# Kernel tuning notes

Hardware: AMD Instinct MI355X
Metric: run time of the kernel (lower is better)

## Reference

```python
import jax, jax.numpy as jnp
import numpy as np

DIM = 512
L = 4096
B, H, W = 8, 64, 64
EPS = 1e-06
BN_EPS = 1e-05


def setup_inputs() -> dict:
    key = jax.random.key(0)
    ks = jax.random.split(key, 16)
    s = 1.0 / np.sqrt(DIM)
    d = {
        'x': jax.random.normal(ks[0], (B, DIM, H, W), dtype=jnp.float32),
        'pos_emb': jax.random.normal(ks[1], (1, L, DIM), dtype=jnp.float32),
        'Wq': jax.random.uniform(ks[2], (DIM, DIM), jnp.float32, -s, s),
        'bq': jax.random.uniform(ks[3], (DIM,), jnp.float32, -s, s),
        'Wk': jax.random.uniform(ks[4], (DIM, DIM), jnp.float32, -s, s),
        'bk': jax.random.uniform(ks[5], (DIM,), jnp.float32, -s, s),
        'Wv': jax.random.uniform(ks[6], (DIM, DIM), jnp.float32, -s, s),
        'bv': jax.random.uniform(ks[7], (DIM,), jnp.float32, -s, s),
        'Wq1': jax.random.uniform(ks[8], (DIM, DIM), jnp.float32, -s, s),
        'bq1': jax.random.uniform(ks[9], (DIM,), jnp.float32, -s, s),
        'Wk1': jax.random.uniform(ks[10], (DIM, DIM), jnp.float32, -s, s),
        'bk1': jax.random.uniform(ks[11], (DIM,), jnp.float32, -s, s),
        'gamma': jax.random.normal(ks[12], (1,), jnp.float32) * 0.1,
        'bn_weight': jnp.ones((DIM,), jnp.float32),
        'bn_bias': jnp.zeros((DIM,), jnp.float32),
    }
    return d


def reference(x, pos_emb, Wq, bq, Wk, bk, Wv, bv, Wq1, bq1, Wk1, bk1, gamma, bn_weight, bn_bias):
    Bb, C, Hh, Ww = x.shape
    # [B,C,H,W] -> [B, L, C] tokens
    xs = x.transpose(0, 2, 3, 1).reshape(Bb, Hh * Ww, C) + pos_emb
    Q = jax.nn.relu(xs @ Wq.T + bq)   # kernel_fun = ReLU
    K = jax.nn.relu(xs @ Wk.T + bk)
    V = xs @ Wv.T + bv
    Q1 = xs @ Wq1.T + bq1
    K1 = xs @ Wk1.T + bk1
    # torch einsum 'blc,bcc,bl->blc' uses only diag(KV); compute it directly:
    # diagKV[b,c] = sum_l K[b,l,c] * V[b,l,c]
    diagKV = jnp.einsum('blc,blc->bc', K, V)
    Ksum = K.sum(axis=1)  # == K^T summed over last axis, [B,C]
    Z = 1.0 / jnp.einsum('blc,bc->bl', Q, Ksum + EPS)
    result = Q * diagKV[:, None, :] * Z[:, :, None]  # [B,L,C]
    # channel-softmax attention: softmax over last dim of Q1^T @ K1, [B,C,C]
    mid = jax.nn.softmax(jnp.einsum('blc,bld->bcd', Q1, K1), axis=-1)
    result = result @ mid  # [B,L,C]
    xs = xs + gamma * result
    y = xs.transpose(0, 2, 1).reshape(Bb, C, Hh, Ww)
    # BatchNorm2d in training mode (fresh module): batch stats, biased variance
    mean = y.mean(axis=(0, 2, 3))
    var = y.var(axis=(0, 2, 3))
    yn = (y - mean[None, :, None, None]) * jax.lax.rsqrt(var + BN_EPS)[None, :, None, None]
    yn = yn * bn_weight[None, :, None, None] + bn_bias[None, :, None, None]
    return jax.nn.relu(yn)
```

## Files before the change

### kernel.cpp

```cpp
#include <hip/hip_runtime.h>
#include <stdint.h>

typedef float f32x4 __attribute__((ext_vector_type(4)));
typedef short bf16x8 __attribute__((ext_vector_type(8)));

__device__ __forceinline__ float bf2f(unsigned short h){
  union { unsigned int u; float f; } v; v.u = ((unsigned int)h) << 16; return v.f;
}
__device__ __forceinline__ unsigned short f2bf(float f){
  union { float f; unsigned int u; } v; v.f = f;
  return (unsigned short)((v.u + 0x7fffu + ((v.u >> 16) & 1u)) >> 16);
}

typedef __attribute__((address_space(1))) const unsigned int ga_u32;
typedef __attribute__((address_space(3))) unsigned int ls_u32;
__device__ __forceinline__ void async_load16(const void* g, void* l){
  __builtin_amdgcn_global_load_lds((ga_u32*)g, (ls_u32*)l, 16, 0, 0);
}

#define CFENCE() asm volatile("" ::: "memory")
#define SB0() __builtin_amdgcn_sched_barrier(0)

__global__ __launch_bounds__(256) void k_prep_all(
    const float* __restrict__ w0, const float* __restrict__ w1,
    const float* __restrict__ w2, const float* __restrict__ w3,
    const float* __restrict__ w4,
    const float* __restrict__ b0, const float* __restrict__ b1,
    const float* __restrict__ b2, const float* __restrict__ b3,
    const float* __restrict__ b4,
    unsigned short* __restrict__ wbf, float* __restrict__ bias5,
    unsigned short* __restrict__ wq1x2)
{
  const int bid = blockIdx.x;
  const int t = threadIdx.x;
  if (bid < 5120){
    int slot = bid >> 10;
    int i = (bid & 1023) * 256 + t;
    const float* w = (slot == 0) ? w0 : (slot == 1) ? w1 :
                     (slot == 2) ? w2 : (slot == 3) ? w3 : w4;
    wbf[(size_t)slot * 262144 + i] = f2bf(w[i]);
  } else if (bid < 5130){
    int i = (bid - 5120) * 256 + t;
    int s = i >> 9, r = i & 511;
    const float* b = (s == 0) ? b0 : (s == 1) ? b1 : (s == 2) ? b2 :
                     (s == 3) ? b3 : b4;
    bias5[i] = b[r];
  } else {
    int e = bid - 5130;
    #pragma unroll
    for (int rep = 0; rep < 2; rep++){
      int idx = rep*256 + t;
      unsigned short v = f2bf(w3[e*512 + idx]);
      wq1x2[(size_t)e*1024 + idx] = v;
      wq1x2[(size_t)e*1024 + 512 + idx] = v;
    }
  }
}

__global__ __launch_bounds__(256) void k_build_xs(
    const float* __restrict__ x, const float* __restrict__ pos,
    unsigned short* __restrict__ xsb, unsigned short* __restrict__ xsT,
    float* __restrict__ svec)
{
  __shared__ float tile[64][65];
  __shared__ unsigned short tile2[64][72];
  __shared__ float sred[256];
  const int lt = blockIdx.x, ct = blockIdx.y;
  const int t = threadIdx.x;
  const int rr = t >> 3, c8 = (t & 7) * 8;
  float pr[16];
  #pragma unroll
  for (int pass = 0; pass < 2; pass++){
    int gl = lt*64 + rr + pass*32;
    f32x4 p0 = *(const f32x4*)(pos + (size_t)gl * 512 + ct*64 + c8);
    f32x4 p1 = *(const f32x4*)(pos + (size_t)gl * 512 + ct*64 + c8 + 4);
    #pragma unroll
    for (int s = 0; s < 4; s++){ pr[pass*8+s] = p0[s]; pr[pass*8+4+s] = p1[s]; }
  }
  for (int b = 0; b < 8; b++){
    #pragma unroll
    for (int pass = 0; pass < 2; pass++){
      int r = rr + pass * 32;
      const float* src = x + ((size_t)b * 512 + ct*64 + r) * 4096 + lt*64 + c8;
      f32x4 v0 = *(const f32x4*)src;
      f32x4 v1 = *(const f32x4*)(src + 4);
      #pragma unroll
      for (int s = 0; s < 4; s++){ tile[r][c8+s] = v0[s]; tile[r][c8+4+s] = v1[s]; }
    }
    __syncthreads();
    #pragma unroll
    for (int pass = 0; pass < 2; pass++){
      int ll = rr + pass * 32;
      int gl = lt*64 + ll;
      bf16x8 hv;
      #pragma unroll
      for (int s = 0; s < 8; s++){
        unsigned short h = f2bf(tile[c8+s][ll] + pr[pass*8+s]);
        hv[s] = (short)h;
        tile2[c8+s][ll] = h;
      }
      *(bf16x8*)(xsb + ((size_t)b * 4096 + gl) * 512 + ct*64 + c8) = hv;
    }
    __syncthreads();
    #pragma unroll
    for (int rep = 0; rep < 2; rep++){
      int c = rep*32 + (t >> 3);
      int l0 = (t & 7) * 8;
      bf16x8 v = *(const bf16x8*)&tile2[c][l0];
      *(bf16x8*)(xsT + ((size_t)b * 512 + ct*64 + c) * 4096 + lt*64 + l0) = v;
    }
    {
      const int c = t & 63, lq = t >> 6;
      float s_ = 0.f;
      #pragma unroll
      for (int j = 0; j < 16; j++) s_ += bf2f(tile2[c][lq*16 + j]);
      sred[t] = s_;
      __syncthreads();
      if (t < 64){
        float ss = sred[t] + sred[t+64] + sred[t+128] + sred[t+192];
        atomicAdd(&svec[b*512 + ct*64 + t], ss);
      }
    }
    __syncthreads();
  }
}

__global__ __launch_bounds__(256) void k_z(
    const unsigned short* __restrict__ Qb, const float* __restrict__ ksum,
    float* __restrict__ Z)
{
  const int row = blockIdx.x * 4 + (threadIdx.x >> 6);
  const int lane = threadIdx.x & 63;
  const int b = row >> 12;
  bf16x8 q = *(const bf16x8*)(Qb + (size_t)row * 512 + lane * 8);
  f32x4 k0 = *(const f32x4*)(ksum + b*512 + lane*8);
  f32x4 k1 = *(const f32x4*)(ksum + b*512 + lane*8 + 4);
  float den = 0.f;
  #pragma unroll
  for (int s = 0; s < 4; s++) den += bf2f((unsigned short)q[s])   * (k0[s] + 1e-6f);
  #pragma unroll
  for (int s = 0; s < 4; s++) den += bf2f((unsigned short)q[4+s]) * (k1[s] + 1e-6f);
  #pragma unroll
  for (int m = 1; m < 64; m <<= 1) den += __shfl_xor(den, m);
  if (lane == 0) Z[row] = 1.0f / den;
}

__global__ __launch_bounds__(64) void k_softmax(
    const float* __restrict__ S, unsigned short* __restrict__ mid)
{
  const size_t row = blockIdx.x;
  const int lane = threadIdx.x;
  const float* p = S + row * 512 + lane * 8;
  f32x4 v0 = *(const f32x4*)p, v1 = *(const f32x4*)(p + 4);
  float mx = v0[0];
  #pragma unroll
  for (int s = 1; s < 4; s++) mx = fmaxf(mx, v0[s]);
  #pragma unroll
  for (int s = 0; s < 4; s++) mx = fmaxf(mx, v1[s]);
  #pragma unroll
  for (int m = 1; m < 64; m <<= 1) mx = fmaxf(mx, __shfl_xor(mx, m));
  float e[8]; float sum = 0.f;
  #pragma unroll
  for (int s = 0; s < 4; s++){ e[s]   = __expf(v0[s] - mx); sum += e[s]; }
  #pragma unroll
  for (int s = 0; s < 4; s++){ e[4+s] = __expf(v1[s] - mx); sum += e[4+s]; }
  #pragma unroll
  for (int m = 1; m < 64; m <<= 1) sum += __shfl_xor(sum, m);
  float inv = 1.0f / sum;
  bf16x8 hv;
  #pragma unroll
  for (int s = 0; s < 8; s++) hv[s] = (short)f2bf(e[s] * inv);
  *(bf16x8*)(mid + row * 512 + lane * 8) = hv;
}

__global__ __launch_bounds__(256) void k_transpose_scale(
    const unsigned short* __restrict__ in, const float* __restrict__ diag,
    unsigned short* __restrict__ out)
{
  __shared__ float tile[64][65];
  const int rt = blockIdx.x, ct = blockIdx.y, z = blockIdx.z;
  const unsigned short* src = in  + (size_t)z * 262144;
  unsigned short*       dst = out + (size_t)z * 262144;
  const int t = threadIdx.x;
  const int rr = t >> 3, c8 = (t & 7) * 8;
  #pragma unroll
  for (int pass = 0; pass < 2; pass++){
    int r = rr + pass * 32;
    bf16x8 v = *(const bf16x8*)(src + (size_t)(rt*64 + r) * 512 + ct*64 + c8);
    #pragma unroll
    for (int s = 0; s < 8; s++) tile[r][c8+s] = bf2f((unsigned short)v[s]);
  }
  __syncthreads();
  f32x4 dg0 = *(const f32x4*)(diag + z*512 + rt*64 + c8);
  f32x4 dg1 = *(const f32x4*)(diag + z*512 + rt*64 + c8 + 4);
  #pragma unroll
  for (int pass = 0; pass < 2; pass++){
    int c = rr + pass * 32;
    bf16x8 hv;
    #pragma unroll
    for (int s = 0; s < 4; s++) hv[s]   = (short)f2bf(tile[c8+s][c]   * dg0[s]);
    #pragma unroll
    for (int s = 0; s < 4; s++) hv[4+s] = (short)f2bf(tile[c8+4+s][c] * dg1[s]);
    *(bf16x8*)(dst + (size_t)(ct*64 + c) * 512 + rt*64 + c8) = hv;
  }
}

#define GEMM_PRE()                                                            \
  const int tid = threadIdx.x;                                                \
  const int lane = tid & 63;                                                  \
  const int wave = tid >> 6;                                                  \
  const int wm = wave >> 1, wn = wave & 1;                                    \
  size_t aoff[4], boff[4]; int ldsq[4];                                       \
  _Pragma("unroll")                                                           \
  for (int i = 0; i < 4; i++){                                                \
    int qq = i*4 + wave;                                                      \
    int ch = qq*64 + lane;                                                    \
    int m  = ch >> 3, p = ch & 7;                                             \
    int lc = p ^ (m & 7);                                                     \
    aoff[i] = (size_t)(m0 + m) * K + lc*8;                                    \
    boff[i] = (size_t)m * K + lc*8;                                           \
    ldsq[i] = qq * 1024;                                                      \
  }                                                                           \
  f32x4 acc[4][4];                                                            \
  const f32x4 vzero = {0.f,0.f,0.f,0.f};                                      \
  _Pragma("unroll")                                                           \
  for (int i = 0; i < 4; i++)                                                 \
    _Pragma("unroll")                                                         \
    for (int j = 0; j < 4; j++) acc[i][j] = vzero;                            \
  int arow[4], brow[4];                                                       \
  _Pragma("unroll")                                                           \
  for (int f = 0; f < 4; f++){                                                \
    arow[f] = (wm*64 + f*16 + (lane & 15)) * 64;                              \
    brow[f] = (wn*64 + f*16 + (lane & 15)) * 64;                              \
  }                                                                           \
  const int kg = lane >> 4;                                                   \
  const int l7 = lane & 7;                                                    \
  const int l15 = lane & 15;

#define GEMM_STAGE2(buf, kt, BB)                                              \
  _Pragma("unroll")                                                           \
  for (int i = 0; i < 4; i++){                                                \
    async_load16(Ae + aoff[i] + (kt)*64, (char*)&smem[(buf)*8192] + ldsq[i]); \
    async_load16((BB) + boff[i] + (kt)*64, (char*)&smem[16384 + (buf)*8192] + ldsq[i]); \
  }

#define GEMM_COMPUTE2(buf, ACC)                                               \
  _Pragma("unroll")                                                           \
  for (int ks = 0; ks < 2; ks++){                                             \
    bf16x8 a[4], b[4];                                                        \
    const int pa = (ks*4 + kg) ^ l7;                                          \
    _Pragma("unroll")                                                         \
    for (int f = 0; f < 4; f++){                                              \
      a[f] = *(const bf16x8*)&smem[(buf)*8192 + arow[f] + pa*8];              \
      b[f] = *(const bf16x8*)&smem[16384 + (buf)*8192 + brow[f] + pa*8];      \
    }                                                                         \
    _Pragma("unroll")                                                         \
    for (int i = 0; i < 4; i++)                                               \
      _Pragma("unroll")                                                       \
      for (int j = 0; j < 4; j++)                                             \
        (ACC)[i][j] = __builtin_amdgcn_mfma_f32_16x16x32_bf16(a[i], b[j], (ACC)[i][j], 0, 0, 0); \
  }

#define GEMM_KLOOP2(nkt, BB)                                                  \
  GEMM_STAGE2(0, 0, BB);                                                      \
  __syncthreads();                                                            \
  { int cur = 0;                                                              \
    for (int kt = 0; kt < (nkt); kt++){                                       \
      if (kt + 1 < (nkt)) { GEMM_STAGE2(cur ^ 1, kt + 1, BB); }               \
      GEMM_COMPUTE2(cur, acc);                                                \
      __syncthreads();                                                        \
      cur ^= 1;                                                               \
    } }

__global__ __launch_bounds__(256, 2) void k_mega(
    const unsigned short* __restrict__ A,
    const unsigned short* __restrict__ xsT,
    const unsigned short* __restrict__ W,
    const float* __restrict__ bias5,
    const float* __restrict__ svec,
    unsigned short* __restrict__ Qb,
    unsigned short* __restrict__ Gstk,
    float* __restrict__ diag, float* __restrict__ ksum,
    float* __restrict__ uvec, float* __restrict__ wvec)
{
  __shared__ unsigned short smem[32768];
  const int bid = blockIdx.x;
  const int xcd = bid & 7, local = bid >> 3;

  if (local < 32){
    const int gw = xcd*32 + local;
    const int part = gw & 1;
    const int ntile = (gw >> 1) & 3;
    const int mtile = (gw >> 3) & 3;
    const int z = gw >> 5;
    const int m0 = mtile * 128, n0 = ntile * 128;
    const int K = 4096;
    const unsigned short* Ae = xsT + (size_t)z * 2097152 + part * 2048;
    const unsigned short* Be = Ae + (size_t)n0 * 4096;

    GEMM_PRE();
    GEMM_KLOOP2(32, Be);

    #pragma unroll
    for (int j = 0; j < 4; j++){
      const int cl = wn*64 + j*16 + l15;
      #pragma unroll
      for (int i = 0; i < 4; i++){
        const int rb = wm*64 + i*16 + kg*4;
        #pragma unroll
        for (int q = 0; q < 4; q++)
          smem[(rb + q)*136 + cl] = f2bf(acc[i][j][q]);
      }
    }
    __syncthreads();
    #pragma unroll
    for (int rep = 0; rep < 8; rep++){
      const int rl = rep*16 + (tid >> 4);
      const int c0 = (tid & 15) * 8;
      bf16x8 v = *(const bf16x8*)&smem[rl*136 + c0];
      *(bf16x8*)(Gstk + (size_t)z*524288 + (size_t)(m0 + rl)*1024 + part*512 + n0 + c0) = v;
    }
    return;
  }

  if (local >= 288){
    const int uwid = xcd*2 + (local - 288);
    const int sel = uwid & 1, b = uwid >> 1;
    const int t = threadIdx.x;
    float* sv = (float*)(void*)smem;
    sv[t] = svec[b*512 + t]; sv[t+256] = svec[b*512 + t + 256];
    __syncthreads();
    const unsigned short* Wp = W + (size_t)(3 + sel) * 262144;
    float* o = sel ? wvec : uvec;
    #pragma unroll
    for (int rep = 0; rep < 2; rep++){
      int e = rep*256 + t;
      const unsigned short* row = Wp + (size_t)e * 512;
      float acc_ = 0.f;
      for (int ch = 0; ch < 64; ch++){
        bf16x8 v = *(const bf16x8*)(row + ch*8);
        #pragma unroll
        for (int j = 0; j < 8; j++) acc_ += bf2f((unsigned short)v[j]) * sv[ch*8+j];
      }
      o[b*512 + e] = acc_;
    }
    return;
  }

  const int pw = xcd*256 + (local - 32);
  const int mtile = pw >> 3;
  const int unit  = pw & 7;
  const int m0 = mtile * 128;
  const int K = 512;
  const unsigned short* Ae = A;

  int mode, cb;
  const unsigned short* BeK; const unsigned short* BeV = W;
  if (unit < 4){ mode = 0; cb = unit*128;     BeK = W + (size_t)cb * 512; }
  else         { mode = 1; cb = (unit-4)*128; BeK = W + 262144 + (size_t)cb * 512;
                                              BeV = W + 524288 + (size_t)cb * 512; }

  GEMM_PRE();

  if (mode == 1){
    const int bz = mtile >> 5;
    GEMM_STAGE2(0, 0, BeK);
    __syncthreads();
    int cur = 0;
    for (int kt = 0; kt < 8; kt++){
      if (kt < 7) { GEMM_STAGE2(cur ^ 1, kt + 1, BeK); }
      else        { GEMM_STAGE2(cur ^ 1, 0, BeV); }
      GEMM_COMPUTE2(cur, acc);
      __syncthreads();
      cur ^= 1;
    }
    GEMM_STAGE2(cur ^ 1, 1, BeV);
    unsigned int kpk[4][4][2];
    #pragma unroll
    for (int j = 0; j < 4; j++){
      const int cj = cb + wn*64 + j*16 + l15;
      const float bb = bias5[512 + cj];
      float ks_ = 0.f;
      #pragma unroll
      for (int i = 0; i < 4; i++){
        #pragma unroll
        for (int h = 0; h < 2; h++){
          float v0 = acc[i][j][2*h]   + bb; v0 = v0 > 0.f ? v0 : 0.f;
          float v1 = acc[i][j][2*h+1] + bb; v1 = v1 > 0.f ? v1 : 0.f;
          unsigned short h0 = f2bf(v0), h1 = f2bf(v1);
          kpk[i][j][h] = (unsigned)h0 | ((unsigned)h1 << 16);
          ks_ += bf2f(h0) + bf2f(h1);
        }
        acc[i][j] = vzero;
      }
      ks_ += __shfl_xor(ks_, 16);
      ks_ += __shfl_xor(ks_, 32);
      if (lane < 16) atomicAdd(&ksum[bz*512 + cj], ks_);
    }
    for (int kt = 0; kt < 8; kt++){
      if (kt >= 1 && kt < 7) { GEMM_STAGE2(cur ^ 1, kt + 1, BeV); }
      GEMM_COMPUTE2(cur, acc);
      __syncthreads();
      cur ^= 1;
    }
    #pragma unroll
    for (int j = 0; j < 4; j++){
      const int cj = cb + wn*64 + j*16 + l15;
      const float bb = bias5[1024 + cj];
      float dv = 0.f;
      #pragma unroll
      for (int i = 0; i < 4; i++){
        #pragma unroll
        for (int h = 0; h < 2; h++){
          float v0 = bf2f(f2bf(acc[i][j][2*h]   + bb));
          float v1 = bf2f(f2bf(acc[i][j][2*h+1] + bb));
          dv += bf2f((unsigned short)(kpk[i][j][h] & 0xffffu)) * v0
              + bf2f((unsigned short)(kpk[i][j][h] >> 16))     * v1;
        }
      }
      dv += __shfl_xor(dv, 16);
      dv += __shfl_xor(dv, 32);
      if (lane < 16) atomicAdd(&diag[bz*512 + cj], dv);
    }
    return;
  }

  GEMM_KLOOP2(8, BeK);

  #pragma unroll
  for (int j = 0; j < 4; j++){
    const int cl = wn*64 + j*16 + l15;
    const float bb = bias5[cb + cl];
    #pragma unroll
    for (int i = 0; i < 4; i++){
      const int rb = wm*64 + i*16 + kg*4;
      #pragma unroll
      for (int q = 0; q < 4; q++){
        float v = acc[i][j][q] + bb; v = v > 0.f ? v : 0.f;
        smem[(rb + q)*136 + cl] = f2bf(v);
      }
    }
  }
  __syncthreads();
  #pragma unroll
  for (int rep = 0; rep < 8; rep++){
    const int rl = rep*16 + (tid >> 4);
    const int c0 = (tid & 15) * 8;
    bf16x8 v = *(const bf16x8*)&smem[rl*136 + c0];
    *(bf16x8*)(Qb + (size_t)(m0 + rl) * 512 + cb + c0) = v;
  }
}

__global__ __launch_bounds__(256) void gemm_P(
    const unsigned short* __restrict__ Wq1x2,
    const unsigned short* __restrict__ Gstk,
    unsigned short* __restrict__ P)
{
  __shared__ unsigned short smem[32768];
  const int bid = blockIdx.x;
  const int wgid = (bid & 7) * 16 + (bid >> 3);
  const int z = wgid >> 4;
  const int mtile = (wgid >> 2) & 3, ntile = wgid & 3;
  const int m0 = mtile * 128, n0 = ntile * 128;
  const int K = 1024;
  const unsigned short* Ae = Wq1x2;
  const unsigned short* Be = Gstk + (size_t)z * 524288 + (size_t)n0 * 1024;

  GEMM_PRE();
  GEMM_KLOOP2(16, Be);

  #pragma unroll
  for (int j = 0; j < 4; j++){
    const int cl = wn*64 + j*16 + l15;
    #pragma unroll
    for (int i = 0; i < 4; i++){
      const int rb = wm*64 + i*16 + kg*4;
      #pragma unroll
      for (int q = 0; q < 4; q++)
        smem[(rb + q)*136 + cl] = f2bf(acc[i][j][q]);
    }
  }
  __syncthreads();
  #pragma unroll
  for (int rep = 0; rep < 8; rep++){
    const int rl = rep*16 + (tid >> 4);
    const int c0 = (tid & 15) * 8;
    bf16x8 v = *(const bf16x8*)&smem[rl*136 + c0];
    *(bf16x8*)(P + (size_t)z * 262144 + (size_t)(m0 + rl) * 512 + n0 + c0) = v;
  }
}

__global__ __launch_bounds__(256) void gemm_S(
    const unsigned short* __restrict__ P,
    const unsigned short* __restrict__ Wk1b,
    const float* __restrict__ bias5,
    const float* __restrict__ u, const float* __restrict__ w,
    float* __restrict__ Sf)
{
  __shared__ unsigned short smem[32768];
  const int bid = blockIdx.x;
  const int wgid = (bid & 7) * 16 + (bid >> 3);
  const int z = wgid >> 4;
  const int mtile = (wgid >> 2) & 3, ntile = wgid & 3;
  const int m0 = mtile * 128, n0 = ntile * 128;
  const int K = 512;
  const unsigned short* Ae = P + (size_t)z * 262144;
  const unsigned short* Be = Wk1b + (size_t)n0 * 512;

  GEMM_PRE();
  GEMM_KLOOP2(8, Be);

  #pragma unroll
  for (int j = 0; j < 4; j++){
    int cd = n0 + wn*64 + j*16 + l15;
    float bkv = bias5[2048 + cd];
    float wv  = w[z*512 + cd] + 4096.0f * bkv;
    #pragma unroll
    for (int i = 0; i < 4; i++){
      int r = m0 + wm*64 + i*16 + kg*4;
      #pragma unroll
      for (int q = 0; q < 4; q++){
        int rr = r + q;
        float uq  = u[z*512 + rr];
        float bqv = bias5[1536 + rr];
        Sf[(size_t)z * 262144 + (size_t)rr * 512 + cd] =
            acc[i][j][q] + uq * bkv + bqv * wv;
      }
    }
  }
}

#define G8_PRE(AE)                                                            \
  const int t = threadIdx.x;                                                  \
  const int lane = t & 63;                                                    \
  const int wave = t >> 6;                                                    \
  const int wm = wave >> 2, wn = wave & 3;                                    \
  const int l15 = lane & 15, kg = lane >> 4;                                  \
  const int lcw = ((t & 7) ^ ((t >> 3) & 7)) * 8;                             \
  const unsigned short* a_src = (AE) + (size_t)(m0 + (t >> 3)) * 512 + lcw;   \
  f32x4 acc[8][4];                                                            \
  const f32x4 vzero = {0.f,0.f,0.f,0.f};                                      \
  _Pragma("unroll")                                                           \
  for (int i = 0; i < 8; i++)                                                 \
    _Pragma("unroll")                                                         \
    for (int j = 0; j < 4; j++) acc[i][j] = vzero;                            \
  bf16x8 af[4][2], bf[4][2];

#define STAGE_A(D,H,TT) do{                                                   \
  async_load16(a_src + (H)*65536 + (TT)*64,                                   \
               (char*)smem + ((D)*16384 + (H)*8192 + t*8)*2);                 \
  async_load16(a_src + (H)*65536 + 32768 + (TT)*64,                           \
               (char*)smem + ((D)*16384 + (H)*8192 + 4096 + t*8)*2);          \
}while(0)

#define STAGE_B(D,H,TT) do{                                                   \
  async_load16(b_src + (H)*65536 + (TT)*64,                                   \
               (char*)smem + (32768 + (D)*16384 + (H)*8192 + t*8)*2);         \
  async_load16(b_src + (H)*65536 + 32768 + (TT)*64,                           \
               (char*)smem + (32768 + (D)*16384 + (H)*8192 + 4096 + t*8)*2);  \
}while(0)

#define READ_A(D, MH) do{                                                     \
  _Pragma("unroll")                                                           \
  for (int mfl = 0; mfl < 4; ++mfl){                                          \
    const int rl = ((MH)*4 + mfl)*16 + l15;                                   \
    _Pragma("unroll")                                                         \
    for (int ks = 0; ks < 2; ++ks){                                           \
      const int ck = (ks*4 + kg) ^ (rl & 7);                                  \
      af[mfl][ks] = *(const bf16x8*)&smem[(D)*16384 + wm*8192 + rl*64 + ck*8];\
    }                                                                         \
  }                                                                           \
}while(0)

#define READ_B(D, NP) do{                                                     \
  _Pragma("unroll")                                                           \
  for (int nfl = 0; nfl < 2; ++nfl){                                          \
    const int nf = (NP)*2 + nfl;                                              \
    const int rbl = (wn & 1)*64 + nf*16 + l15;                                \
    _Pragma("unroll")                                                         \
    for (int ks = 0; ks < 2; ++ks){                                           \
      const int ck = (ks*4 + kg) ^ (rbl & 7);                                 \
      bf[nf][ks] = *(const bf16x8*)&smem[32768 + (D)*16384 + (wn>>1)*8192 + rbl*64 + ck*8]; \
    }                                                                         \
  }                                                                           \
}while(0)

#define QUAD(MH, NP)                                                          \
  _Pragma("unroll")                                                           \
  for (int mfl = 0; mfl < 4; ++mfl)                                           \
    _Pragma("unroll")                                                         \
    for (int nfl = 0; nfl < 2; ++nfl)                                         \
      _Pragma("unroll")                                                       \
      for (int ks = 0; ks < 2; ++ks)                                          \
        acc[(MH)*4+mfl][(NP)*2+nfl] = __builtin_amdgcn_mfma_f32_16x16x32_bf16(\
            af[mfl][ks], bf[(NP)*2+nfl][ks], acc[(MH)*4+mfl][(NP)*2+nfl], 0,0,0);

#define PH_MID()  CFENCE(); __builtin_amdgcn_s_barrier();                     \
  __builtin_amdgcn_s_setprio(1); SB0()
#define PH_END()  SB0(); __builtin_amdgcn_s_setprio(0); CFENCE();             \
  __builtin_amdgcn_s_barrier(); CFENCE()
#define PH_END_VM4() SB0(); __builtin_amdgcn_s_setprio(0);                    \
  asm volatile("s_waitcnt vmcnt(4)" ::: "memory");                            \
  __builtin_amdgcn_s_barrier(); CFENCE()
#define PH_END_VM0() SB0(); __builtin_amdgcn_s_setprio(0);                    \
  asm volatile("s_waitcnt vmcnt(0)" ::: "memory");                            \
  __builtin_amdgcn_s_barrier(); CFENCE()

#define G8_KLOOP()                                                            \
  STAGE_A(0,0,0); STAGE_A(0,1,0); STAGE_B(0,0,0); STAGE_B(0,1,0);             \
  STAGE_B(1,0,1); STAGE_B(1,1,1);                                             \
  asm volatile("s_waitcnt vmcnt(4)" ::: "memory");                            \
  __builtin_amdgcn_s_barrier(); CFENCE();                                     \
  for (int it = 0; it < 3; ++it){                                             \
    const int t1 = 2*it + 1, t2 = 2*it + 2, t3 = 2*it + 3;                    \
    READ_A(0,0); READ_B(0,0); STAGE_A(1,0,t1);                                \
    PH_MID(); QUAD(0,0); PH_END();                                            \
    READ_B(0,1); STAGE_A(1,1,t1);                                             \
    PH_MID(); QUAD(0,1); PH_END();                                            \
    READ_A(0,1); STAGE_B(0,0,t2);                                             \
    PH_MID(); QUAD(1,0); PH_END();                                            \
    STAGE_A(0,0,t2);                                                          \
    PH_MID(); QUAD(1,1); PH_END_VM4();                                        \
    READ_A(1,0); READ_B(1,0); STAGE_A(0,1,t2);                                \
    PH_MID(); QUAD(0,0); PH_END();                                            \
    READ_B(1,1); STAGE_B(0,1,t2);                                             \
    PH_MID(); QUAD(0,1); PH_END();                                            \
    READ_A(1,1); STAGE_B(1,0,t3);                                             \
    PH_MID(); QUAD(1,0); PH_END();                                            \
    STAGE_B(1,1,t3);                                                          \
    PH_MID(); QUAD(1,1); PH_END_VM4();                                        \
  }                                                                           \
  { READ_A(0,0); READ_B(0,0); STAGE_A(1,0,7);                                 \
    PH_MID(); QUAD(0,0); PH_END();                                            \
    READ_B(0,1); STAGE_A(1,1,7);                                              \
    PH_MID(); QUAD(0,1); PH_END();                                            \
    READ_A(0,1);                                                              \
    PH_MID(); QUAD(1,0); PH_END();                                            \
    PH_MID(); QUAD(1,1); PH_END_VM0();                                        \
    READ_A(1,0); READ_B(1,0);                                                 \
    PH_MID(); QUAD(0,0); PH_END();                                            \
    READ_B(1,1);                                                              \
    PH_MID(); QUAD(0,1); PH_END();                                            \
    READ_A(1,1);                                                              \
    PH_MID(); QUAD(1,0); PH_END();                                            \
    PH_MID(); QUAD(1,1); PH_END(); }

__global__ __launch_bounds__(512, 2) void gemm8_res(
    const unsigned short* __restrict__ A,
    const unsigned short* __restrict__ Bt,
    const float* __restrict__ Zp,
    unsigned short* __restrict__ outh,
    const float* __restrict__ gamma_p,
    float* __restrict__ bnS, float* __restrict__ bnQ)
{
  __shared__ unsigned short smem[65536];
  __shared__ float zbuf[256];
  const int bid = blockIdx.x;
  const int wgid = (bid & 7) * 32 + (bid >> 3);
  const int mtile = wgid >> 1;
  const int ntile = wgid & 1;
  const int m0 = mtile * 256;
  const int nc0 = ntile * 256;

  G8_PRE(A);
  const unsigned short* b_src =
      Bt + (size_t)(mtile >> 4) * 262144 + (size_t)(nc0 + (t >> 3)) * 512 + lcw;

  G8_KLOOP();

  const float g = gamma_p[0];
  __syncthreads();
  if (t < 256) zbuf[t] = Zp[m0 + t];
  __syncthreads();
  #pragma unroll
  for (int nf = 0; nf < 4; nf++){
    int cl = wn*64 + nf*16 + l15;
    #pragma unroll
    for (int mf = 0; mf < 8; mf++){
      int rbase = wm*128 + mf*16 + kg*4;
      #pragma unroll
      for (int q = 0; q < 4; q++){
        int rl = rbase + q;
        smem[rl*256 + (cl ^ (((rl >> 2) & 3) << 4))] =
            f2bf(g * zbuf[rl] * acc[mf][nf][q]);
      }
    }
  }
  __syncthreads();
  float sc[8] = {0.f,0.f,0.f,0.f,0.f,0.f,0.f,0.f};
  float sq[8] = {0.f,0.f,0.f,0.f,0.f,0.f,0.f,0.f};
  const int c0 = (t & 31) * 8;
  #pragma unroll
  for (int rep = 0; rep < 16; rep++){
    int rl = rep*16 + (t >> 5);
    bf16x8 ga = *(const bf16x8*)&smem[rl*256 + (c0 ^ (((rl >> 2) & 3) << 4))];
    size_t gidx = (size_t)(m0 + rl) * 512 + nc0 + c0;
    bf16x8 xv = *(const bf16x8*)(outh + gidx);
    bf16x8 yv;
    #pragma unroll
    for (int j = 0; j < 8; j++){
      float y = bf2f((unsigned short)xv[j]) + bf2f((unsigned short)ga[j]);
      yv[j] = (short)f2bf(y);
      sc[j] += y; sq[j] += y * y;
    }
    *(bf16x8*)(outh + gidx) = yv;
  }
  __syncthreads();
  float* red = (float*)(void*)smem;
  const int tg = t >> 5;
  f32x4 s0 = {sc[0],sc[1],sc[2],sc[3]}, s1 = {sc[4],sc[5],sc[6],sc[7]};
  f32x4 q0 = {sq[0],sq[1],sq[2],sq[3]}, q1 = {sq[4],sq[5],sq[6],sq[7]};
  *(f32x4*)&red[tg*256 + c0]        = s0;  *(f32x4*)&red[tg*256 + c0 + 4]        = s1;
  *(f32x4*)&red[4096 + tg*256 + c0] = q0;  *(f32x4*)&red[4096 + tg*256 + c0 + 4] = q1;
  __syncthreads();
  if (t < 256){
    float ss = 0.f, qq = 0.f;
    #pragma unroll
    for (int gg = 0; gg < 16; gg++){
      ss += red[gg*256 + t];
      qq += red[4096 + gg*256 + t];
    }
    atomicAdd(&bnS[nc0 + t], ss);
    atomicAdd(&bnQ[nc0 + t], qq);
  }
}

__global__ __launch_bounds__(256) void k_bn_finalize(
    const unsigned short* __restrict__ y, const float* __restrict__ bnS,
    const float* __restrict__ bnQ, const float* __restrict__ bnw,
    const float* __restrict__ bnb, float* __restrict__ out)
{
  __shared__ float tile[64][65];
  __shared__ float scale_s[64], shift_s[64];
  const int lt = blockIdx.x, ct = blockIdx.y, b = blockIdx.z;
  const int t = threadIdx.x;
  if (t < 64){
    int c = ct*64 + t;
    float s = bnS[c], q = bnQ[c];
    float mean = s * (1.0f / 32768.0f);
    float var  = q * (1.0f / 32768.0f) - mean * mean;
    float inv  = rsqrtf(var + 1e-5f);
    float scv  = bnw[c] * inv;
    scale_s[t] = scv;
    shift_s[t] = bnb[c] - mean * scv;
  }
  const int rr = t >> 3, c8 = (t & 7) * 8;
  #pragma unroll
  for (int pass = 0; pass < 2; pass++){
    int l = rr + pass * 32;
    bf16x8 v = *(const bf16x8*)(y + ((size_t)b * 4096 + lt*64 + l) * 512 + ct*64 + c8);
    #pragma unroll
    for (int s = 0; s < 8; s++) tile[l][c8+s] = bf2f((unsigned short)v[s]);
  }
  __syncthreads();
  #pragma unroll
  for (int pass = 0; pass < 2; pass++){
    int c = rr + pass * 32;
    float scv = scale_s[c], sh = shift_s[c];
    f32x4 o0, o1;
    #pragma unroll
    for (int s = 0; s < 4; s++){
      float v = tile[c8+s][c] * scv + sh;     o0[s] = v > 0.f ? v : 0.f;
      float w = tile[c8+4+s][c] * scv + sh;   o1[s] = w > 0.f ? w : 0.f;
    }
    float* dp = out + ((size_t)b * 512 + ct*64 + c) * 4096 + lt*64 + c8;
    *(f32x4*)dp = o0;
    *(f32x4*)(dp + 4) = o1;
  }
}

extern "C" void kernel_launch(void* const* d_in, const int* in_sizes, int n_in,
                              void* d_out, int out_size, void* d_ws, size_t ws_size,
                              hipStream_t stream)
{
  const float* x    = (const float*)d_in[0];
  const float* pos  = (const float*)d_in[1];
  const float* Wq   = (const float*)d_in[2];
  const float* bq   = (const float*)d_in[3];
  const float* Wk   = (const float*)d_in[4];
  const float* bk   = (const float*)d_in[5];
  const float* Wv   = (const float*)d_in[6];
  const float* bv   = (const float*)d_in[7];
  const float* Wq1  = (const float*)d_in[8];
  const float* bq1  = (const float*)d_in[9];
  const float* Wk1  = (const float*)d_in[10];
  const float* bk1  = (const float*)d_in[11];
  const float* gam  = (const float*)d_in[12];
  const float* bnw  = (const float*)d_in[13];
  const float* bnb  = (const float*)d_in[14];
  float* out = (float*)d_out;
  char* ws = (char*)d_ws;

  const size_t MB = 1ull << 20;
  const size_t OFF_XSB  = 0;
  const size_t OFF_QB   = 32*MB;
  const size_t OFF_XST  = 64*MB;
  const size_t OFF_GSTK = 96*MB;
  const size_t OFF_PBF  = 104*MB;
  const size_t OFF_SF   = 108*MB;
  const size_t OFF_MIDB = 116*MB;
  const size_t OFF_MIDT = 120*MB;
  const size_t OFF_WBF  = 124*MB;
  const size_t OFF_WQ2  = 127*MB;
  const size_t OFF_B5   = 128*MB + 512*1024;
  const size_t OFF_UV   = 129*MB;
  const size_t OFF_WV   = OFF_UV + 16384;
  const size_t OFF_Z    = OFF_WV + 16384;
  const size_t OFF_DIAG = 130*MB;
  const size_t OFF_KSUM = OFF_DIAG + 16384;
  const size_t OFF_BNS  = OFF_KSUM + 16384;
  const size_t OFF_BNQ  = OFF_BNS + 2048;
  const size_t OFF_SV   = OFF_BNQ + 2048;
  const size_t ZERO_LEN = 16384 + 16384 + 2048 + 2048 + 16384;
  const size_t WS_NEED  = OFF_SV + 16384;
  if (ws_size < WS_NEED) return;

  unsigned short* xsb  = (unsigned short*)(ws + OFF_XSB);
  unsigned short* Qb   = (unsigned short*)(ws + OFF_QB);
  unsigned short* xsT  = (unsigned short*)(ws + OFF_XST);
  unsigned short* Gstk = (unsigned short*)(ws + OFF_GSTK);
  unsigned short* Pbf  = (unsigned short*)(ws + OFF_PBF);
  float*          Sf   = (float*)(ws + OFF_SF);
  unsigned short* midb = (unsigned short*)(ws + OFF_MIDB);
  unsigned short* midT = (unsigned short*)(ws + OFF_MIDT);
  unsigned short* wbf  = (unsigned short*)(ws + OFF_WBF);
  unsigned short* wq1x2= (unsigned short*)(ws + OFF_WQ2);
  float* bias5 = (float*)(ws + OFF_B5);
  float* uvec = (float*)(ws + OFF_UV);
  float* wvec = (float*)(ws + OFF_WV);
  float* Zp   = (float*)(ws + OFF_Z);
  float* diag = (float*)(ws + OFF_DIAG);
  float* ksum = (float*)(ws + OFF_KSUM);
  float* bnS  = (float*)(ws + OFF_BNS);
  float* bnQ  = (float*)(ws + OFF_BNQ);
  float* svec = (float*)(ws + OFF_SV);

  hipMemsetAsync(ws + OFF_DIAG, 0, ZERO_LEN, stream);

  k_prep_all<<<dim3(5642), 256, 0, stream>>>(Wq, Wk, Wv, Wq1, Wk1,
                                             bq, bk, bv, bq1, bk1,
                                             wbf, bias5, wq1x2);

  k_build_xs<<<dim3(64, 8), 256, 0, stream>>>(x, pos, xsb, xsT, svec);

  k_mega<<<dim3(2320), 256, 0, stream>>>(xsb, xsT, wbf, bias5, svec,
                                         Qb, Gstk, diag, ksum, uvec, wvec);

  k_z<<<dim3(8192), 256, 0, stream>>>(Qb, ksum, Zp);

  gemm_P<<<dim3(128), 256, 0, stream>>>(wq1x2, Gstk, Pbf);
  gemm_S<<<dim3(128), 256, 0, stream>>>(Pbf, wbf + 4*262144, bias5, uvec, wvec, Sf);

  k_softmax<<<dim3(4096), 64, 0, stream>>>(Sf, midb);
  k_transpose_scale<<<dim3(8, 8, 8), 256, 0, stream>>>(midb, diag, midT);

  gemm8_res<<<dim3(256), 512, 0, stream>>>(Qb, midT, Zp, xsb, gam, bnS, bnQ);

  k_bn_finalize<<<dim3(64, 8, 8), 256, 0, stream>>>(xsb, bnS, bnQ, bnw, bnb, out);
}
```

Measured before the change: 219.4 us.

## Fuse Z computation into gemm_P launch and retile residual GEMM to 128x128

```diff
diff --git a/kernel.cpp b/kernel.cpp
--- a/kernel.cpp
+++ b/kernel.cpp
@@ -19,7 +19,6 @@
 }
 
 #define CFENCE() asm volatile("" ::: "memory")
-#define SB0() __builtin_amdgcn_sched_barrier(0)
 
 __global__ __launch_bounds__(256) void k_prep_all(
     const float* __restrict__ w0, const float* __restrict__ w1,
@@ -123,26 +122,6 @@
     }
     __syncthreads();
   }
-}
-
-__global__ __launch_bounds__(256) void k_z(
-    const unsigned short* __restrict__ Qb, const float* __restrict__ ksum,
-    float* __restrict__ Z)
-{
-  const int row = blockIdx.x * 4 + (threadIdx.x >> 6);
-  const int lane = threadIdx.x & 63;
-  const int b = row >> 12;
-  bf16x8 q = *(const bf16x8*)(Qb + (size_t)row * 512 + lane * 8);
-  f32x4 k0 = *(const f32x4*)(ksum + b*512 + lane*8);
-  f32x4 k1 = *(const f32x4*)(ksum + b*512 + lane*8 + 4);
-  float den = 0.f;
-  #pragma unroll
-  for (int s = 0; s < 4; s++) den += bf2f((unsigned short)q[s])   * (k0[s] + 1e-6f);
-  #pragma unroll
-  for (int s = 0; s < 4; s++) den += bf2f((unsigned short)q[4+s]) * (k1[s] + 1e-6f);
-  #pragma unroll
-  for (int m = 1; m < 64; m <<= 1) den += __shfl_xor(den, m);
-  if (lane == 0) Z[row] = 1.0f / den;
 }
 
 __global__ __launch_bounds__(64) void k_softmax(
@@ -451,13 +430,35 @@
   }
 }
 
-__global__ __launch_bounds__(256) void gemm_P(
+__global__ __launch_bounds__(256) void k_pz(
     const unsigned short* __restrict__ Wq1x2,
     const unsigned short* __restrict__ Gstk,
-    unsigned short* __restrict__ P)
+    unsigned short* __restrict__ P,
+    const unsigned short* __restrict__ Qb,
+    const float* __restrict__ ksum,
+    float* __restrict__ Z)
 {
   __shared__ unsigned short smem[32768];
   const int bid = blockIdx.x;
+
+  if (bid >= 128){
+    const int row = (bid - 128) * 4 + ((int)threadIdx.x >> 6);
+    const int lane = threadIdx.x & 63;
+    const int b = row >> 12;
+    bf16x8 q = *(const bf16x8*)(Qb + (size_t)row * 512 + lane * 8);
+    f32x4 k0 = *(const f32x4*)(ksum + b*512 + lane*8);
+    f32x4 k1 = *(const f32x4*)(ksum + b*512 + lane*8 + 4);
+    float den = 0.f;
+    #pragma unroll
+    for (int s = 0; s < 4; s++) den += bf2f((unsigned short)q[s])   * (k0[s] + 1e-6f);
+    #pragma unroll
+    for (int s = 0; s < 4; s++) den += bf2f((unsigned short)q[4+s]) * (k1[s] + 1e-6f);
+    #pragma unroll
+    for (int m = 1; m < 64; m <<= 1) den += __shfl_xor(den, m);
+    if (lane == 0) Z[row] = 1.0f / den;
+    return;
+  }
+
   const int wgid = (bid & 7) * 16 + (bid >> 3);
   const int z = wgid >> 4;
   const int mtile = (wgid >> 2) & 3, ntile = wgid & 3;
@@ -530,122 +531,7 @@
   }
 }
 
-#define G8_PRE(AE)                                                            \
-  const int t = threadIdx.x;                                                  \
-  const int lane = t & 63;                                                    \
-  const int wave = t >> 6;                                                    \
-  const int wm = wave >> 2, wn = wave & 3;                                    \
-  const int l15 = lane & 15, kg = lane >> 4;                                  \
-  const int lcw = ((t & 7) ^ ((t >> 3) & 7)) * 8;                             \
-  const unsigned short* a_src = (AE) + (size_t)(m0 + (t >> 3)) * 512 + lcw;   \
-  f32x4 acc[8][4];                                                            \
-  const f32x4 vzero = {0.f,0.f,0.f,0.f};                                      \
-  _Pragma("unroll")                                                           \
-  for (int i = 0; i < 8; i++)                                                 \
-    _Pragma("unroll")                                                         \
-    for (int j = 0; j < 4; j++) acc[i][j] = vzero;                            \
-  bf16x8 af[4][2], bf[4][2];
-
-#define STAGE_A(D,H,TT) do{                                                   \
-  async_load16(a_src + (H)*65536 + (TT)*64,                                   \
-               (char*)smem + ((D)*16384 + (H)*8192 + t*8)*2);                 \
-  async_load16(a_src + (H)*65536 + 32768 + (TT)*64,                           \
-               (char*)smem + ((D)*16384 + (H)*8192 + 4096 + t*8)*2);          \
-}while(0)
-
-#define STAGE_B(D,H,TT) do{                                                   \
-  async_load16(b_src + (H)*65536 + (TT)*64,                                   \
-               (char*)smem + (32768 + (D)*16384 + (H)*8192 + t*8)*2);         \
-  async_load16(b_src + (H)*65536 + 32768 + (TT)*64,                           \
-               (char*)smem + (32768 + (D)*16384 + (H)*8192 + 4096 + t*8)*2);  \
-}while(0)
-
-#define READ_A(D, MH) do{                                                     \
-  _Pragma("unroll")                                                           \
-  for (int mfl = 0; mfl < 4; ++mfl){                                          \
-    const int rl = ((MH)*4 + mfl)*16 + l15;                                   \
-    _Pragma("unroll")                                                         \
-    for (int ks = 0; ks < 2; ++ks){                                           \
-      const int ck = (ks*4 + kg) ^ (rl & 7);                                  \
-      af[mfl][ks] = *(const bf16x8*)&smem[(D)*16384 + wm*8192 + rl*64 + ck*8];\
-    }                                                                         \
-  }                                                                           \
-}while(0)
-
-#define READ_B(D, NP) do{                                                     \
-  _Pragma("unroll")                                                           \
-  for (int nfl = 0; nfl < 2; ++nfl){                                          \
-    const int nf = (NP)*2 + nfl;                                              \
-    const int rbl = (wn & 1)*64 + nf*16 + l15;                                \
-    _Pragma("unroll")                                                         \
-    for (int ks = 0; ks < 2; ++ks){                                           \
-      const int ck = (ks*4 + kg) ^ (rbl & 7);                                 \
-      bf[nf][ks] = *(const bf16x8*)&smem[32768 + (D)*16384 + (wn>>1)*8192 + rbl*64 + ck*8]; \
-    }                                                                         \
-  }                                                                           \
-}while(0)
-
-#define QUAD(MH, NP)                                                          \
-  _Pragma("unroll")                                                           \
-  for (int mfl = 0; mfl < 4; ++mfl)                                           \
-    _Pragma("unroll")                                                         \
-    for (int nfl = 0; nfl < 2; ++nfl)                                         \
-      _Pragma("unroll")                                                       \
-      for (int ks = 0; ks < 2; ++ks)                                          \
-        acc[(MH)*4+mfl][(NP)*2+nfl] = __builtin_amdgcn_mfma_f32_16x16x32_bf16(\
-            af[mfl][ks], bf[(NP)*2+nfl][ks], acc[(MH)*4+mfl][(NP)*2+nfl], 0,0,0);
-
-#define PH_MID()  CFENCE(); __builtin_amdgcn_s_barrier();                     \
-  __builtin_amdgcn_s_setprio(1); SB0()
-#define PH_END()  SB0(); __builtin_amdgcn_s_setprio(0); CFENCE();             \
-  __builtin_amdgcn_s_barrier(); CFENCE()
-#define PH_END_VM4() SB0(); __builtin_amdgcn_s_setprio(0);                    \
-  asm volatile("s_waitcnt vmcnt(4)" ::: "memory");                            \
-  __builtin_amdgcn_s_barrier(); CFENCE()
-#define PH_END_VM0() SB0(); __builtin_amdgcn_s_setprio(0);                    \
-  asm volatile("s_waitcnt vmcnt(0)" ::: "memory");                            \
-  __builtin_amdgcn_s_barrier(); CFENCE()
-
-#define G8_KLOOP()                                                            \
-  STAGE_A(0,0,0); STAGE_A(0,1,0); STAGE_B(0,0,0); STAGE_B(0,1,0);             \
-  STAGE_B(1,0,1); STAGE_B(1,1,1);                                             \
-  asm volatile("s_waitcnt vmcnt(4)" ::: "memory");                            \
-  __builtin_amdgcn_s_barrier(); CFENCE();                                     \
-  for (int it = 0; it < 3; ++it){                                             \
-    const int t1 = 2*it + 1, t2 = 2*it + 2, t3 = 2*it + 3;                    \
-    READ_A(0,0); READ_B(0,0); STAGE_A(1,0,t1);                                \
-    PH_MID(); QUAD(0,0); PH_END();                                            \
-    READ_B(0,1); STAGE_A(1,1,t1);                                             \
-    PH_MID(); QUAD(0,1); PH_END();                                            \
-    READ_A(0,1); STAGE_B(0,0,t2);                                             \
-    PH_MID(); QUAD(1,0); PH_END();                                            \
-    STAGE_A(0,0,t2);                                                          \
-    PH_MID(); QUAD(1,1); PH_END_VM4();                                        \
-    READ_A(1,0); READ_B(1,0); STAGE_A(0,1,t2);                                \
-    PH_MID(); QUAD(0,0); PH_END();                                            \
-    READ_B(1,1); STAGE_B(0,1,t2);                                             \
-    PH_MID(); QUAD(0,1); PH_END();                                            \
-    READ_A(1,1); STAGE_B(1,0,t3);                                             \
-    PH_MID(); QUAD(1,0); PH_END();                                            \
-    STAGE_B(1,1,t3);                                                          \
-    PH_MID(); QUAD(1,1); PH_END_VM4();                                        \
-  }                                                                           \
-  { READ_A(0,0); READ_B(0,0); STAGE_A(1,0,7);                                 \
-    PH_MID(); QUAD(0,0); PH_END();                                            \
-    READ_B(0,1); STAGE_A(1,1,7);                                              \
-    PH_MID(); QUAD(0,1); PH_END();                                            \
-    READ_A(0,1);                                                              \
-    PH_MID(); QUAD(1,0); PH_END();                                            \
-    PH_MID(); QUAD(1,1); PH_END_VM0();                                        \
-    READ_A(1,0); READ_B(1,0);                                                 \
-    PH_MID(); QUAD(0,0); PH_END();                                            \
-    READ_B(1,1);                                                              \
-    PH_MID(); QUAD(0,1); PH_END();                                            \
-    READ_A(1,1);                                                              \
-    PH_MID(); QUAD(1,0); PH_END();                                            \
-    PH_MID(); QUAD(1,1); PH_END(); }
-
-__global__ __launch_bounds__(512, 2) void gemm8_res(
+__global__ __launch_bounds__(256, 2) void gemm_res2(
     const unsigned short* __restrict__ A,
     const unsigned short* __restrict__ Bt,
     const float* __restrict__ Zp,
@@ -653,47 +539,46 @@
     const float* __restrict__ gamma_p,
     float* __restrict__ bnS, float* __restrict__ bnQ)
 {
-  __shared__ unsigned short smem[65536];
-  __shared__ float zbuf[256];
+  __shared__ unsigned short smem[32768];
+  __shared__ float zbuf[128];
   const int bid = blockIdx.x;
-  const int wgid = (bid & 7) * 32 + (bid >> 3);
-  const int mtile = wgid >> 1;
-  const int ntile = wgid & 1;
-  const int m0 = mtile * 256;
-  const int nc0 = ntile * 256;
-
-  G8_PRE(A);
-  const unsigned short* b_src =
-      Bt + (size_t)(mtile >> 4) * 262144 + (size_t)(nc0 + (t >> 3)) * 512 + lcw;
-
-  G8_KLOOP();
+  const int wgid = (bid & 7) * 128 + (bid >> 3);
+  const int mtile = wgid >> 2;
+  const int ntile = wgid & 3;
+  const int m0 = mtile * 128;
+  const int nc0 = ntile * 128;
+  const int K = 512;
+  const unsigned short* Ae = A;
+  const unsigned short* Be =
+      Bt + (size_t)(mtile >> 5) * 262144 + (size_t)nc0 * 512;
+
+  GEMM_PRE();
+  GEMM_KLOOP2(8, Be);
 
   const float g = gamma_p[0];
+  if (tid < 128) zbuf[tid] = Zp[m0 + tid];
   __syncthreads();
-  if (t < 256) zbuf[t] = Zp[m0 + t];
-  __syncthreads();
-  #pragma unroll
-  for (int nf = 0; nf < 4; nf++){
-    int cl = wn*64 + nf*16 + l15;
-    #pragma unroll
-    for (int mf = 0; mf < 8; mf++){
-      int rbase = wm*128 + mf*16 + kg*4;
+  #pragma unroll
+  for (int j = 0; j < 4; j++){
+    const int cl = wn*64 + j*16 + l15;
+    #pragma unroll
+    for (int i = 0; i < 4; i++){
+      const int rb = wm*64 + i*16 + kg*4;
       #pragma unroll
       for (int q = 0; q < 4; q++){
-        int rl = rbase + q;
-        smem[rl*256 + (cl ^ (((rl >> 2) & 3) << 4))] =
-            f2bf(g * zbuf[rl] * acc[mf][nf][q]);
+        const int rl = rb + q;
+        smem[rl*136 + cl] = f2bf(g * zbuf[rl] * acc[i][j][q]);
       }
     }
   }
   __syncthreads();
   float sc[8] = {0.f,0.f,0.f,0.f,0.f,0.f,0.f,0.f};
   float sq[8] = {0.f,0.f,0.f,0.f,0.f,0.f,0.f,0.f};
-  const int c0 = (t & 31) * 8;
-  #pragma unroll
-  for (int rep = 0; rep < 16; rep++){
-    int rl = rep*16 + (t >> 5);
-    bf16x8 ga = *(const bf16x8*)&smem[rl*256 + (c0 ^ (((rl >> 2) & 3) << 4))];
+  const int c0 = (tid & 15) * 8;
+  #pragma unroll
+  for (int rep = 0; rep < 8; rep++){
+    const int rl = rep*16 + (tid >> 4);
+    bf16x8 ga = *(const bf16x8*)&smem[rl*136 + c0];
     size_t gidx = (size_t)(m0 + rl) * 512 + nc0 + c0;
     bf16x8 xv = *(const bf16x8*)(outh + gidx);
     bf16x8 yv;
@@ -707,21 +592,21 @@
   }
   __syncthreads();
   float* red = (float*)(void*)smem;
-  const int tg = t >> 5;
+  const int tg = tid >> 4;
   f32x4 s0 = {sc[0],sc[1],sc[2],sc[3]}, s1 = {sc[4],sc[5],sc[6],sc[7]};
   f32x4 q0 = {sq[0],sq[1],sq[2],sq[3]}, q1 = {sq[4],sq[5],sq[6],sq[7]};
-  *(f32x4*)&red[tg*256 + c0]        = s0;  *(f32x4*)&red[tg*256 + c0 + 4]        = s1;
-  *(f32x4*)&red[4096 + tg*256 + c0] = q0;  *(f32x4*)&red[4096 + tg*256 + c0 + 4] = q1;
+  *(f32x4*)&red[tg*128 + c0]        = s0;  *(f32x4*)&red[tg*128 + c0 + 4]        = s1;
+  *(f32x4*)&red[2048 + tg*128 + c0] = q0;  *(f32x4*)&red[2048 + tg*128 + c0 + 4] = q1;
   __syncthreads();
-  if (t < 256){
+  if (tid < 128){
     float ss = 0.f, qq = 0.f;
     #pragma unroll
     for (int gg = 0; gg < 16; gg++){
-      ss += red[gg*256 + t];
-      qq += red[4096 + gg*256 + t];
-    }
-    atomicAdd(&bnS[nc0 + t], ss);
-    atomicAdd(&bnQ[nc0 + t], qq);
+      ss += red[gg*128 + tid];
+      qq += red[2048 + gg*128 + tid];
+    }
+    atomicAdd(&bnS[nc0 + tid], ss);
+    atomicAdd(&bnQ[nc0 + tid], qq);
   }
 }
 
@@ -846,15 +731,14 @@
   k_mega<<<dim3(2320), 256, 0, stream>>>(xsb, xsT, wbf, bias5, svec,
                                          Qb, Gstk, diag, ksum, uvec, wvec);
 
-  k_z<<<dim3(8192), 256, 0, stream>>>(Qb, ksum, Zp);
-
-  gemm_P<<<dim3(128), 256, 0, stream>>>(wq1x2, Gstk, Pbf);
+  k_pz<<<dim3(8320), 256, 0, stream>>>(wq1x2, Gstk, Pbf, Qb, ksum, Zp);
+
   gemm_S<<<dim3(128), 256, 0, stream>>>(Pbf, wbf + 4*262144, bias5, uvec, wvec, Sf);
 
   k_softmax<<<dim3(4096), 64, 0, stream>>>(Sf, midb);
   k_transpose_scale<<<dim3(8, 8, 8), 256, 0, stream>>>(midb, diag, midT);
 
-  gemm8_res<<<dim3(256), 512, 0, stream>>>(Qb, midT, Zp, xsb, gam, bnS, bnQ);
+  gemm_res2<<<dim3(1024), 256, 0, stream>>>(Qb, midT, Zp, xsb, gam, bnS, bnQ);
 
   k_bn_finalize<<<dim3(64, 8, 8), 256, 0, stream>>>(xsb, bnS, bnQ, bnw, bnb, out);
 }
```

Result: no change. 220.4 us (+0.4%).
